# Kernel optimization log

Hardware: AMD Instinct MI355X
Metric: run time of the kernel (lower is better)

Reference implementation:

```python
import jax, jax.numpy as jnp
import numpy as np

RADIUS = 10  # watermark_radius
EPS = 1e-5   # BatchNorm eps

def _conv(x, w, b, g, be, m, v):
    # Conv2d 3x3 pad 1 + BatchNorm(eval) + ReLU, NCHW
    y = jax.lax.conv_general_dilated(x, w, (1, 1), 'SAME',
                                     dimension_numbers=('NCHW', 'OIHW', 'NCHW'))
    y = y + b[None, :, None, None]
    y = g[None, :, None, None] * (y - m[None, :, None, None]) * jax.lax.rsqrt(v + EPS)[None, :, None, None] + be[None, :, None, None]
    return jax.nn.relu(y)

def _watermark_indices(C, H, W, L, r):
    # Replicates the (channel, i, j) iteration order of the torch loop.
    chs, ys, xs = [], [], []
    cy0, cx0 = H // 2, W // 2
    for c in range(C):
        for i in range(-r, r + 1):
            for j in range(-r, r + 1):
                if len(chs) >= L:
                    return np.array(chs), np.array(ys), np.array(xs)
                y, x = cy0 + i, cx0 + j
                if 0 <= y < H and 0 <= x < W and i * i + j * j <= r * r:
                    chs.append(c); ys.append(y); xs.append(x)
    return np.array(chs), np.array(ys), np.array(xs)

def setup_inputs() -> dict:
    key = jax.random.key(0)
    ks = jax.random.split(key, 8)
    B, Cc, H, W, L = 16, 64, 256, 256, 256
    s = 0.05  # weight scale for numerical stability
    inp = {
        'image': jax.random.normal(ks[0], (B, 3, H, W), jnp.float32),
        'message': jax.random.uniform(ks[1], (B, L), jnp.float32),
        'w0': jax.random.normal(ks[2], (Cc, 3, 3, 3), jnp.float32) * s,
        'b0': jnp.zeros((Cc,), jnp.float32),
        'g0': jnp.ones((Cc,), jnp.float32),
        'be0': jnp.zeros((Cc,), jnp.float32),
        'm0': jnp.zeros((Cc,), jnp.float32),
        'v0': jnp.ones((Cc,), jnp.float32),
        'wk': jax.random.normal(ks[3], (3, Cc, Cc, 3, 3), jnp.float32) * s,
        'bk': jnp.zeros((3, Cc), jnp.float32),
        'gk': jnp.ones((3, Cc), jnp.float32),
        'bek': jnp.zeros((3, Cc), jnp.float32),
        'mk': jnp.zeros((3, Cc), jnp.float32),
        'vk': jnp.ones((3, Cc), jnp.float32),
        'wa': jax.random.normal(ks[4], (Cc, Cc + 3 + L, 3, 3), jnp.float32) * s,
        'ba': jnp.zeros((Cc,), jnp.float32),
        'ga': jnp.ones((Cc,), jnp.float32),
        'bea': jnp.zeros((Cc,), jnp.float32),
        'ma': jnp.zeros((Cc,), jnp.float32),
        'va': jnp.ones((Cc,), jnp.float32),
        'wf': jax.random.normal(ks[5], (3, Cc, 1, 1), jnp.float32) * s,
        'bf': jnp.zeros((3,), jnp.float32),
    }
    return inp

def reference(image, message, w0, b0, g0, be0, m0, v0,
              wk, bk, gk, bek, mk, vk,
              wa, ba, ga, bea, ma, va, wf, bf):
    B, _, H, W = image.shape
    L = message.shape[1]
    # conv stack
    x = _conv(image, w0, b0, g0, be0, m0, v0)
    for t in range(wk.shape[0]):
        x = _conv(x, wk[t], bk[t], gk[t], bek[t], mk[t], vk[t])
    C = x.shape[1]
    # FFT2 over spatial dims
    fft = jnp.fft.fft2(x.astype(jnp.complex64))
    # vectorized tree-ring watermark scatter (precomputed static indices)
    ch, yy, xx = _watermark_indices(C, H, W, L, RADIUS)
    vals = message[:, :ch.shape[0]]                      # [B, L]
    cvals = (vals + 1j * vals).astype(jnp.complex64)     # complex(value, value)
    fft = fft.at[:, ch, yy, xx].set(cvals)
    enc = jnp.fft.ifft2(fft).real.astype(image.dtype)
    # concat [expanded message, encoded, image]
    msg = jnp.broadcast_to(message[:, :, None, None], (B, L, H, W))
    cat = jnp.concatenate([msg, enc, image], axis=1)
    y = _conv(cat, wa, ba, ga, bea, ma, va)
    # final 1x1 conv
    out = jnp.einsum('bchw,oc->bohw', y, wf[:, :, 0, 0]) + bf[None, :, None, None]
    return out
```

## Files before the change

### kernel.cpp

```cpp
#include <hip/hip_runtime.h>
#include <hip/hip_bf16.h>

#define HH 256
#define WW 256
#define NB 16
#define CC 64
#define NL 256
#define HWSZ (HH*WW)
#define EPSV 1e-5f
#define NYK 16
#define YK0 118

using bf16 = __hip_bfloat16;
using short8  = __attribute__((ext_vector_type(8))) short;
using floatx4 = __attribute__((ext_vector_type(4))) float;

__device__ __forceinline__ ushort f2b(float f){
    bf16 h = __float2bfloat16(f);
    union { bf16 h; ushort u; } cv; cv.h = h; return cv.u;
}
__device__ __forceinline__ float b2fu(ushort u){
    union { unsigned int i; float f; } cv; cv.i = ((unsigned int)u) << 16; return cv.f;
}

__global__ void prep_w_k(const float* __restrict__ wk, const float* __restrict__ wa,
                         ushort* __restrict__ wkb2, ushort* __restrict__ wab2)
{
    int i = blockIdx.x*256 + threadIdx.x;
    const int NWK = 3*9*64*64, NWA = 19*2048;
    if (i < NWK) {
        int ci8 = i & 7; int r = i >> 3;
        int lane = r & 63; r >>= 6;
        int mi = r & 3; r >>= 2;
        int g = r % 18; int t = r / 18;
        int q = g / 6, kc2 = (g / 3) & 1, p = g % 3;
        int quad = lane >> 4, n16 = lane & 15;
        int co = mi*16 + n16, ci = kc2*32 + quad*8 + ci8, tap = p*3 + q;
        wkb2[i] = f2b(wk[(((size_t)t*64 + co)*64 + ci)*9 + tap]);
    } else if (i < NWK + NWA) {
        int i2 = i - NWK;
        int ci8 = i2 & 7; int r = i2 >> 3;
        int lane = r & 63; r >>= 6;
        int mi = r & 3; int g = r >> 2;
        int quad = lane >> 4, n16 = lane & 15;
        int co = mi*16 + n16;
        float v = 0.f;
        if (g < 18) {
            int q = g/6, kc2 = (g/3)&1, p = g%3;
            int ci = kc2*32 + quad*8 + ci8, tap = p*3 + q;
            v = wa[((size_t)co*323 + 256 + ci)*9 + tap];
        } else {
            int j = quad*8 + ci8;
            if (j < 27) {
                int ci = j/9, rem = j%9;
                v = wa[((size_t)co*323 + 320 + ci)*9 + rem];
            }
        }
        wab2[i2] = f2b(v);
    }
}

#define LDAF2(DST, G) { const ushort* bp = wbase + (size_t)(G)*2048;           \
    DST[0] = *(const short8*)(bp);                                             \
    DST[1] = *(const short8*)(bp + 512); }

#define MFMA_GRP2(AF, BF, P)                                                   \
    _Pragma("unroll") for (int mi_=0; mi_<2; mi_++) {                          \
      _Pragma("unroll") for (int ni_=0; ni_<4; ni_++)                          \
        acc[mi_][ni_] = __builtin_amdgcn_mfma_f32_16x16x32_bf16(               \
            AF[mi_], BF[ni_+(P)], acc[mi_][ni_], 0, 0, 0); }

__global__ __launch_bounds__(512,4) void conv0_k(
    const float* __restrict__ img, const float* __restrict__ w0,
    const float* __restrict__ bias, const float* __restrict__ gamma,
    const float* __restrict__ beta, const float* __restrict__ mean,
    const float* __restrict__ var, ushort* __restrict__ outp)
{
    __shared__ float s_i[3][18][18];
    __shared__ float s_wv[64*27];
    __shared__ float s_al[64], s_be[64];
    __shared__ ushort __align__(16) s_y[256*72];

    int tid = threadIdx.x;
    int x0 = blockIdx.x*16, y0 = blockIdx.y*16, b = blockIdx.z;
    if (tid < 64) {
        float a = gamma[tid]*rsqrtf(var[tid]+EPSV);
        s_al[tid] = a; s_be[tid] = (bias[tid]-mean[tid])*a + beta[tid];
    }
    for (int c = tid; c < 64*27; c += 512) s_wv[c] = w0[c];
    for (int c = tid; c < 3*18*18; c += 512) {
        int ci = c / 324, pp = c % 324, py = pp/18, px = pp%18;
        int gy = y0-1+py, gx = x0-1+px;
        float v = 0.f;
        if ((unsigned)gy < 256u && (unsigned)gx < 256u)
            v = img[((size_t)b*3 + ci)*HWSZ + gy*256 + gx];
        s_i[ci][py][px] = v;
    }
    __syncthreads();

    int px256 = tid & 255;
    int half  = tid >> 8;
    int ly = px256 >> 4, lx = px256 & 15;
    float xv[27];
    #pragma unroll
    for (int ci=0;ci<3;ci++)
      #pragma unroll
      for (int p=0;p<3;p++)
        #pragma unroll
        for (int q=0;q<3;q++)
            xv[ci*9+p*3+q] = s_i[ci][ly+p][lx+q];

    for (int cc=0; cc<32; cc++) {
        int co = half*32 + cc;
        float a = 0.f;
        #pragma unroll
        for (int j=0;j<27;j++) a += xv[j]*s_wv[co*27+j];
        s_y[px256*72 + co] = f2b(fmaxf(s_al[co]*a + s_be[co], 0.f));
    }
    __syncthreads();
    size_t obase = (size_t)b*HWSZ*64;
    for (int c = tid; c < 256*8; c += 512) {
        int ci8 = c & 7, px = c >> 3;
        int gy = y0 + (px>>4), gx = x0 + (px&15);
        *(uint4*)&outp[obase + (size_t)(gy*256+gx)*64 + ci8*8] =
            *(const uint4*)&s_y[px*72 + ci8*8];
    }
}

__global__ __launch_bounds__(512,4) void convm_k(
    const ushort* __restrict__ in, const ushort* __restrict__ wgt,
    ushort* __restrict__ outp,
    const float* __restrict__ gamma, const float* __restrict__ beta,
    const float* __restrict__ mean,  const float* __restrict__ var,
    const float* __restrict__ bias,  float* __restrict__ plane)
{
    __shared__ ushort __align__(16) s_x[18*18*72];
    __shared__ float s_al[64], s_be[64];

    const int tid = threadIdx.x;
    const int x0 = blockIdx.x*16, y0 = blockIdx.y*16, b = blockIdx.z;

    if (tid < 64) {
        float a = gamma[tid]*rsqrtf(var[tid]+EPSV);
        s_al[tid] = a; s_be[tid] = (bias[tid]-mean[tid])*a + beta[tid];
    }
    const size_t ibase = (size_t)b*HWSZ*64;
    for (int c = tid; c < 18*18*8; c += 512) {
        int ci8 = c & 7, pp = c >> 3;
        int px = pp % 18, py = pp / 18;
        int gy = y0-1+py, gx = x0-1+px;
        uint4 v = make_uint4(0,0,0,0);
        if ((unsigned)gy < 256u && (unsigned)gx < 256u)
            v = *(const uint4*)&in[ibase + (size_t)(gy*256+gx)*64 + ci8*8];
        *(uint4*)&s_x[(py*18+px)*72 + ci8*8] = v;
    }
    __syncthreads();

    const int lane = tid & 63, wv = tid >> 6;
    const int wid = wv & 3, grp = wv >> 2;
    const int n16 = lane & 15, quad = lane >> 4;
    const ushort* wbase = wgt + (size_t)lane*8 + (size_t)grp*1024;

    floatx4 acc[2][4];
    #pragma unroll
    for (int mi=0;mi<2;mi++)
      #pragma unroll
      for (int ni=0;ni<4;ni++)
        #pragma unroll
        for (int r=0;r<4;r++) acc[mi][ni][r] = 0.f;

    short8 afA[2], afB[2], bfA[6], bfB[6];

    LDAF2(afA, 0);
    #pragma unroll
    for (int rr=0; rr<6; rr++)
        bfA[rr] = *(const short8*)&s_x[((wid*4+rr)*18 + n16)*72 + quad*8];

    #pragma unroll
    for (int g=0; g<18; g++) {
        const int p = g % 3, j = g / 3;
        if (g+1 < 18) {
            if (g & 1) { LDAF2(afA, g+1); } else { LDAF2(afB, g+1); }
        }
        if (p == 0 && j+1 < 6) {
            const int nq = (j+1) >> 1, nk = (j+1) & 1;
            if (j & 1) {
                #pragma unroll
                for (int rr=0; rr<6; rr++)
                    bfA[rr] = *(const short8*)&s_x[((wid*4+rr)*18 + n16 + nq)*72 + nk*32 + quad*8];
            } else {
                #pragma unroll
                for (int rr=0; rr<6; rr++)
                    bfB[rr] = *(const short8*)&s_x[((wid*4+rr)*18 + n16 + nq)*72 + nk*32 + quad*8];
            }
        }
        if (g & 1) { if (j & 1) { MFMA_GRP2(afB, bfB, p) } else { MFMA_GRP2(afB, bfA, p) } }
        else       { if (j & 1) { MFMA_GRP2(afA, bfB, p) } else { MFMA_GRP2(afA, bfA, p) } }
    }
    __syncthreads();

    ushort* s_y = s_x;
    #pragma unroll
    for (int mi=0;mi<2;mi++)
      #pragma unroll
      for (int ni=0;ni<4;ni++) {
        int ami = grp*2 + mi;
        int px = (wid*4+ni)*16 + n16;
        int cob = ami*16 + quad*4;
        ushort u[4];
        #pragma unroll
        for (int r=0;r<4;r++) {
            float y = fmaxf(s_al[cob+r]*acc[mi][ni][r] + s_be[cob+r], 0.f);
            u[r] = f2b(y);
            if (plane && ami==0 && quad==0 && r==0)
                plane[(size_t)b*HWSZ + (y0+wid*4+ni)*256 + x0 + n16] = y;
        }
        uint2 pk; pk.x = (uint)u[0] | ((uint)u[1]<<16); pk.y = (uint)u[2] | ((uint)u[3]<<16);
        *(uint2*)&s_y[px*72 + cob] = pk;
      }
    __syncthreads();
    for (int c = tid; c < 256*8; c += 512) {
        int ci8 = c & 7, px = c >> 3;
        int gy = y0 + (px>>4), gx = x0 + (px&15);
        *(uint4*)&outp[ibase + (size_t)(gy*256+gx)*64 + ci8*8] =
            *(const uint4*)&s_y[px*72 + ci8*8];
    }
}

__global__ __launch_bounds__(512,4) void conva_k(
    const ushort* __restrict__ enc, const float* __restrict__ img,
    const float* __restrict__ dplane, const ushort* __restrict__ wgt,
    const float* __restrict__ gamma, const float* __restrict__ beta,
    const float* __restrict__ mean,  const float* __restrict__ var,
    const float* __restrict__ bias,
    const float* __restrict__ Tb,
    const float* __restrict__ wf, const float* __restrict__ bfv,
    float* __restrict__ outp)
{
    __shared__ ushort __align__(16) s_x[18*18*72];
    __shared__ float s_al[64], s_be[64];
    __shared__ float s_T[64*9];
    __shared__ float s_wf[3*64];
    __shared__ float s_bf[3];

    const int tid = threadIdx.x;
    const int x0 = blockIdx.x*16, y0 = blockIdx.y*16, b = blockIdx.z;

    if (tid < 64) {
        float a = gamma[tid]*rsqrtf(var[tid]+EPSV);
        s_al[tid] = a; s_be[tid] = (bias[tid]-mean[tid])*a + beta[tid];
    }
    if (tid < 192) s_wf[tid] = wf[tid];
    if (tid < 3)   s_bf[tid] = bfv[tid];
    for (int c = tid; c < 64*9; c += 512) s_T[c] = Tb[(size_t)b*576 + c];

    const int lane = tid & 63, wv = tid >> 6;
    const int wid = wv & 3, grp = wv >> 2;
    const int n16 = lane & 15, quad = lane >> 4;
    const ushort* wbase = wgt + (size_t)lane*8 + (size_t)grp*1024;

    const size_t ibase = (size_t)b*HWSZ*64;
    for (int c = tid; c < 18*18*8; c += 512) {
        int ci8 = c & 7, pp = c >> 3;
        int px = pp % 18, py = pp / 18;
        int gy = y0-1+py, gx = x0-1+px;
        uint4 v = make_uint4(0,0,0,0);
        if ((unsigned)gy < 256u && (unsigned)gx < 256u) {
            v = *(const uint4*)&enc[ibase + (size_t)(gy*256+gx)*64 + ci8*8];
            if (ci8 == 0) {
                float d = dplane[(size_t)b*HWSZ + gy*256 + gx];
                ushort nb = f2b(b2fu((ushort)(v.x & 0xffffu)) + d);
                v.x = (v.x & 0xffff0000u) | (uint)nb;
            }
        }
        *(uint4*)&s_x[(py*18+px)*72 + ci8*8] = v;
    }

    short8 bimg[4];
    #pragma unroll
    for (int ni=0; ni<4; ni++) {
        short8 t;
        #pragma unroll
        for (int ci8=0; ci8<8; ci8++) {
            int j = quad*8 + ci8;
            float v = 0.f;
            if (j < 27) {
                int ci = j/9, rem = j%9, p = rem/3, q = rem%3;
                int gy = y0 + wid*4 + ni + p - 1, gx = x0 + n16 + q - 1;
                if ((unsigned)gy < 256u && (unsigned)gx < 256u)
                    v = img[((size_t)b*3 + ci)*HWSZ + gy*256 + gx];
            }
            t[ci8] = (short)f2b(v);
        }
        bimg[ni] = t;
    }
    __syncthreads();

    floatx4 acc[2][4];
    #pragma unroll
    for (int mi=0;mi<2;mi++)
      #pragma unroll
      for (int ni=0;ni<4;ni++)
        #pragma unroll
        for (int r=0;r<4;r++) acc[mi][ni][r] = 0.f;

    short8 afA[2], afB[2], bf[6];

    LDAF2(afA, 0);
    #pragma unroll
    for (int g=0; g<18; g++) {
        const int p = g % 3, j = g / 3;
        if (g & 1) { LDAF2(afA, g+1); } else { LDAF2(afB, g+1); }
        if (p == 0) {
            const int nq = j >> 1, nk = j & 1;
            #pragma unroll
            for (int rr=0; rr<6; rr++)
                bf[rr] = *(const short8*)&s_x[((wid*4+rr)*18 + n16 + nq)*72 + nk*32 + quad*8];
        }
        if (g & 1) { MFMA_GRP2(afB, bf, p) } else { MFMA_GRP2(afA, bf, p) }
    }
    #pragma unroll
    for (int mi=0;mi<2;mi++)
      #pragma unroll
      for (int ni=0;ni<4;ni++)
        acc[mi][ni] = __builtin_amdgcn_mfma_f32_16x16x32_bf16(
            afA[mi], bimg[ni], acc[mi][ni], 0, 0, 0);

    float po[3][4];
    #pragma unroll
    for (int o=0;o<3;o++)
      #pragma unroll
      for (int ni=0;ni<4;ni++) po[o][ni] = 0.f;

    #pragma unroll
    for (int mi=0;mi<2;mi++) {
        int cob = (grp*2 + mi)*16 + quad*4;
        #pragma unroll
        for (int r=0;r<4;r++) {
            int co = cob + r;
            float al = s_al[co], be = s_be[co];
            const float* t = &s_T[co*9];
            float w0f = s_wf[0*64+co], w1f = s_wf[1*64+co], w2f = s_wf[2*64+co];
            #pragma unroll
            for (int ni=0;ni<4;ni++) {
                int h = y0 + wid*4 + ni, w = x0 + n16;
                float tv = t[0];
                if (h==0)   tv -= t[1];
                if (h==255) tv -= t[2];
                if (w==0)   tv -= t[3];
                if (w==255) tv -= t[4];
                if (h==0   && w==0)   tv += t[5];
                if (h==0   && w==255) tv += t[6];
                if (h==255 && w==0)   tv += t[7];
                if (h==255 && w==255) tv += t[8];
                float y = fmaxf(al*(acc[mi][ni][r] + tv) + be, 0.f);
                po[0][ni] += w0f*y; po[1][ni] += w1f*y; po[2][ni] += w2f*y;
            }
        }
    }
    #pragma unroll
    for (int o=0;o<3;o++)
      #pragma unroll
      for (int ni=0;ni<4;ni++) {
        po[o][ni] += __shfl_xor(po[o][ni], 16, 64);
        po[o][ni] += __shfl_xor(po[o][ni], 32, 64);
      }
    __syncthreads();
    float* s_red = (float*)s_x;
    #pragma unroll
    for (int o=0;o<3;o++)
      #pragma unroll
      for (int ni=0;ni<4;ni++)
        if (grp == 1 && quad == o)
            s_red[((wid*3+o)*4+ni)*16 + n16] = po[o][ni];
    __syncthreads();
    #pragma unroll
    for (int o=0;o<3;o++)
      #pragma unroll
      for (int ni=0;ni<4;ni++)
        if (grp == 0 && quad == o) {
            int h = y0 + wid*4 + ni, w = x0 + n16;
            outp[((size_t)b*3 + o)*HWSZ + h*256 + w] =
                po[o][ni] + s_red[((wid*3+o)*4+ni)*16 + n16] + s_bf[o];
        }
}

__global__ __launch_bounds__(256) void msgterm_k(const float* __restrict__ msg,
                                                 const float* __restrict__ wa,
                                                 float* __restrict__ Tbuf)
{
    __shared__ float red[256];
    int b = blockIdx.x, o = blockIdx.y, l = threadIdx.x;
    float m = msg[b*NL + l];
    float wv[9];
    #pragma unroll
    for (int t=0;t<9;t++) wv[t] = wa[((size_t)o*323 + l)*9 + t] * m;
    float comp[9];
    comp[0] = wv[0]+wv[1]+wv[2]+wv[3]+wv[4]+wv[5]+wv[6]+wv[7]+wv[8];
    comp[1] = wv[0]+wv[1]+wv[2];
    comp[2] = wv[6]+wv[7]+wv[8];
    comp[3] = wv[0]+wv[3]+wv[6];
    comp[4] = wv[2]+wv[5]+wv[8];
    comp[5] = wv[0]; comp[6]=wv[2]; comp[7]=wv[6]; comp[8]=wv[8];
    for (int cpi=0;cpi<9;cpi++){
        red[l] = comp[cpi];
        __syncthreads();
        for (int s=128;s>0;s>>=1){ if (l<s) red[l]+=red[l+s]; __syncthreads(); }
        if (l==0) Tbuf[((size_t)b*CC+o)*9+cpi] = red[0];
        __syncthreads();
    }
}

__global__ void build_idx_k(int* __restrict__ idx)
{
    if (threadIdx.x==0 && blockIdx.x==0) {
        int n=0;
        for (int i=-10;i<=10;i++)
            for (int j=-10;j<=10;j++) {
                if (n>=NL) return;
                if (i*i+j*j<=100) { idx[2*n]=128+i; idx[2*n+1]=128+j; n++; }
            }
    }
}

__global__ __launch_bounds__(256) void colA_k(const float* __restrict__ plane,
                                              float* __restrict__ Cbuf)
{
    __shared__ float twc[256], tws[256];
    int t = blockIdx.x, b = blockIdx.y, w = threadIdx.x;
    float sv, cv;
    __sincosf(6.283185307179586f * (float)w / 256.0f, &sv, &cv);
    twc[w]=cv; tws[w]=sv;
    __syncthreads();
    int yk = YK0 + t;
    const float* pb = &plane[(size_t)b*HWSZ];
    int m = 0;
    float fr=0.f, fi=0.f;
    for (int h=0; h<256; h++) {
        float xv = pb[h*256 + w];
        fr += xv*twc[m];
        fi -= xv*tws[m];
        m = (m + yk) & 255;
    }
    float* Cb = &Cbuf[((size_t)(b*NYK + t)*2)*256];
    Cb[w]       = fr;
    Cb[256 + w] = fi;
}

__global__ __launch_bounds__(256) void freqB_k(const float* __restrict__ Cbuf,
                                               const float* __restrict__ msg,
                                               const int* __restrict__ idx,
                                               float* __restrict__ D)
{
    __shared__ float twc[256], tws[256];
    __shared__ float sfr[4], sfi[4];
    int k = blockIdx.x, b = blockIdx.y, w = threadIdx.x;
    float sv, cv;
    __sincosf(6.283185307179586f * (float)w / 256.0f, &sv, &cv);
    twc[w]=cv; tws[w]=sv;
    __syncthreads();
    int yk = idx[2*k], xk = idx[2*k+1];
    int t = yk - YK0;
    const float* Cb = &Cbuf[((size_t)(b*NYK + t)*2)*256];
    float Cr = Cb[w], Ci = Cb[256 + w];
    int ang = (xk*w) & 255;
    float cx = twc[ang], sx = tws[ang];
    float fr = Cr*cx + Ci*sx;
    float fi = Ci*cx - Cr*sx;
    #pragma unroll
    for (int off=32; off>0; off>>=1) {
        fr += __shfl_xor(fr, off, 64);
        fi += __shfl_xor(fi, off, 64);
    }
    if ((w & 63) == 0) { sfr[w>>6] = fr; sfi[w>>6] = fi; }
    __syncthreads();
    if (w == 0) {
        float FR = sfr[0]+sfr[1]+sfr[2]+sfr[3];
        float FI = sfi[0]+sfi[1]+sfi[2]+sfi[3];
        float mv = msg[b*NL + k];
        D[((size_t)b*NL + k)*2 + 0] = mv - FR;
        D[((size_t)b*NL + k)*2 + 1] = mv - FI;
    }
}

__global__ __launch_bounds__(256) void rowC_k(const int* __restrict__ idx,
                                              const float* __restrict__ D,
                                              float* __restrict__ Sbuf)
{
    __shared__ float twc[256], tws[256], dr[256], di[256];
    __shared__ int iy[256], ix[256];
    int t = blockIdx.x, b = blockIdx.y, w = threadIdx.x;
    float sv, cv;
    __sincosf(6.283185307179586f * (float)w / 256.0f, &sv, &cv);
    twc[w]=cv; tws[w]=sv;
    dr[w] = D[((size_t)b*NL + w)*2+0];
    di[w] = D[((size_t)b*NL + w)*2+1];
    iy[w] = idx[2*w]; ix[w] = idx[2*w+1];
    __syncthreads();
    int yk = YK0 + t;
    float Sr=0.f, Si=0.f;
    for (int k=0;k<256;k++) {
        if (iy[k] != yk) continue;
        int ang = (ix[k]*w) & 255;
        float c = twc[ang], s = tws[ang];
        Sr += dr[k]*c - di[k]*s;
        Si += dr[k]*s + di[k]*c;
    }
    float* Sb = &Sbuf[((size_t)(b*NYK + t)*2)*256];
    Sb[w]       = Sr;
    Sb[256 + w] = Si;
}

__global__ __launch_bounds__(256) void applyD_k(const float* __restrict__ Sbuf,
                                                float* __restrict__ dplane)
{
    __shared__ float twc[256], tws[256];
    int h = blockIdx.x, b = blockIdx.y, w = threadIdx.x;
    float sv, cv;
    __sincosf(6.283185307179586f * (float)w / 256.0f, &sv, &cv);
    twc[w]=cv; tws[w]=sv;
    __syncthreads();
    float acc = 0.f;
    #pragma unroll
    for (int t=0;t<NYK;t++) {
        int yk = YK0 + t;
        int ang = (yk*h) & 255;
        float cy = twc[ang], sy = tws[ang];
        const float* Sb = &Sbuf[((size_t)(b*NYK + t)*2)*256];
        acc += cy*Sb[w] - sy*Sb[256 + w];
    }
    dplane[(size_t)b*HWSZ + h*256 + w] = acc * (1.0f/65536.0f);
}

extern "C" void kernel_launch(void* const* d_in, const int* in_sizes, int n_in,
                              void* d_out, int out_size, void* d_ws, size_t ws_size,
                              hipStream_t stream)
{
    const float* image = (const float*)d_in[0];
    const float* msg   = (const float*)d_in[1];
    const float* w0    = (const float*)d_in[2];
    const float* b0    = (const float*)d_in[3];
    const float* g0    = (const float*)d_in[4];
    const float* be0   = (const float*)d_in[5];
    const float* m0    = (const float*)d_in[6];
    const float* v0    = (const float*)d_in[7];
    const float* wk    = (const float*)d_in[8];
    const float* bk    = (const float*)d_in[9];
    const float* gk    = (const float*)d_in[10];
    const float* bek   = (const float*)d_in[11];
    const float* mk    = (const float*)d_in[12];
    const float* vk    = (const float*)d_in[13];
    const float* wa    = (const float*)d_in[14];
    const float* ba    = (const float*)d_in[15];
    const float* ga    = (const float*)d_in[16];
    const float* bea   = (const float*)d_in[17];
    const float* ma    = (const float*)d_in[18];
    const float* va    = (const float*)d_in[19];
    const float* wf    = (const float*)d_in[20];
    const float* bfv   = (const float*)d_in[21];
    float* out = (float*)d_out;

    char* base = (char*)d_ws;
    int*    idx    = (int*)base;
    float*  Dbuf   = (float*)(base + (4<<10));
    float*  Tbuf   = (float*)(base + (40<<10));
    ushort* wkb2   = (ushort*)(base + (128<<10));
    ushort* wab2   = (ushort*)(base + (384<<10));
    float*  Cbuf   = (float*)(base + (512<<10));
    float*  Sbuf   = (float*)(base + ((size_t)1<<20));
    float*  plane  = (float*)(base + ((size_t)2<<20));
    float*  dplane = (float*)(base + ((size_t)7<<20));
    ushort* bufA   = (ushort*)(base + ((size_t)12<<20));

    const size_t perB = (size_t)HWSZ*64*2*2;
    int chunk = 1;
    for (int c = NB; c >= 1; c >>= 1)
        if (((size_t)12<<20) + (size_t)c*perB <= ws_size) { chunk = c; break; }
    ushort* bufB = bufA + (size_t)chunk*HWSZ*64;

    build_idx_k<<<1,64,0,stream>>>(idx);
    msgterm_k<<<dim3(NB,CC),256,0,stream>>>(msg, wa, Tbuf);
    int prep_n = (3*9*64*64 + 19*2048 + 255)/256;
    prep_w_k<<<prep_n,256,0,stream>>>(wk, wa, wkb2, wab2);

    const size_t WL = (size_t)9*64*64;

    for (int cs = 0; cs < NB; cs += chunk) {
        dim3 g(16,16,chunk);
        const float* img_c = image + (size_t)cs*3*HWSZ;

        conv0_k<<<g,512,0,stream>>>(img_c, w0, b0, g0, be0, m0, v0, bufA);
        convm_k<<<g,512,0,stream>>>(bufA, wkb2 + 0*WL, bufB,
            gk+0*CC, bek+0*CC, mk+0*CC, vk+0*CC, bk+0*CC, nullptr);
        convm_k<<<g,512,0,stream>>>(bufB, wkb2 + 1*WL, bufA,
            gk+1*CC, bek+1*CC, mk+1*CC, vk+1*CC, bk+1*CC, nullptr);
        convm_k<<<g,512,0,stream>>>(bufA, wkb2 + 2*WL, bufB,
            gk+2*CC, bek+2*CC, mk+2*CC, vk+2*CC, bk+2*CC, plane);

        colA_k<<<dim3(NYK,chunk),256,0,stream>>>(plane, Cbuf);
        freqB_k<<<dim3(NL,chunk),256,0,stream>>>(Cbuf, msg + (size_t)cs*NL, idx, Dbuf);
        rowC_k<<<dim3(NYK,chunk),256,0,stream>>>(idx, Dbuf, Sbuf);
        applyD_k<<<dim3(HH,chunk),256,0,stream>>>(Sbuf, dplane);

        conva_k<<<g,512,0,stream>>>(bufB, img_c, dplane, wab2,
            ga, bea, ma, va, ba, Tbuf + (size_t)cs*CC*9, wf, bfv,
            out + (size_t)cs*3*HWSZ);
    }
}
```

Measured before the change: 780.4 us.

## Split convm halo load into two channel halves and overlap with MFMA

The convm kernel now loads only the first 32 input channels of the halo tile into LDS before starting compute. The upper 32 channels are prefetched into registers and written to LDS during the first MFMA group. The K-loop order is remapped (GMAP) so the low-channel taps run first, with a barrier at step 6 before the high-channel taps. Halo loads and output stores are also unrolled, and conva_k gets a fast path for interior tiles that skips the border correction terms. This aims to hide global load latency behind MFMA work, at the cost of extra registers for the staged data and an additional barrier.

```diff
diff --git a/kernel.cpp b/kernel.cpp
--- a/kernel.cpp
+++ b/kernel.cpp
@@ -70,6 +70,8 @@
         acc[mi_][ni_] = __builtin_amdgcn_mfma_f32_16x16x32_bf16(               \
             AF[mi_], BF[ni_+(P)], acc[mi_][ni_], 0, 0, 0); }
 
+#define GMAP(G) ((((G)%9)/3)*6 + ((G)/9)*3 + ((G)%3))
+
 __global__ __launch_bounds__(512,4) void conv0_k(
     const float* __restrict__ img, const float* __restrict__ w0,
     const float* __restrict__ bias, const float* __restrict__ gamma,
@@ -145,16 +147,45 @@
         s_al[tid] = a; s_be[tid] = (bias[tid]-mean[tid])*a + beta[tid];
     }
     const size_t ibase = (size_t)b*HWSZ*64;
-    for (int c = tid; c < 18*18*8; c += 512) {
-        int ci8 = c & 7, pp = c >> 3;
+
+    {
+        int c = tid;
+        int ci4 = c & 3; int pp = c >> 2;
         int px = pp % 18, py = pp / 18;
-        int gy = y0-1+py, gx = x0-1+px;
-        uint4 v = make_uint4(0,0,0,0);
-        if ((unsigned)gy < 256u && (unsigned)gx < 256u)
-            v = *(const uint4*)&in[ibase + (size_t)(gy*256+gx)*64 + ci8*8];
-        *(uint4*)&s_x[(py*18+px)*72 + ci8*8] = v;
-    }
-    __syncthreads();
+        #pragma unroll
+        for (int it = 0; it < 3; ++it) {
+            if (c < 1296) {
+                int gy = y0-1+py, gx = x0-1+px;
+                uint4 v = make_uint4(0,0,0,0);
+                if ((unsigned)gy < 256u && (unsigned)gx < 256u)
+                    v = *(const uint4*)&in[ibase + (size_t)(gy*256+gx)*64 + ci4*8];
+                *(uint4*)&s_x[pp*72 + ci4*8] = v;
+            }
+            c += 512; pp += 128; px += 2; py += 7;
+            if (px >= 18) { px -= 18; py += 1; }
+        }
+    }
+    uint4 stgHi[3];
+    {
+        int c = tid;
+        int ci4 = c & 3; int pp = c >> 2;
+        int px = pp % 18, py = pp / 18;
+        #pragma unroll
+        for (int it = 0; it < 3; ++it) {
+            uint4 v = make_uint4(0,0,0,0);
+            if (c < 1296) {
+                int gy = y0-1+py, gx = x0-1+px;
+                if ((unsigned)gy < 256u && (unsigned)gx < 256u)
+                    v = *(const uint4*)&in[ibase + (size_t)(gy*256+gx)*64 + 32 + ci4*8];
+            }
+            stgHi[it] = v;
+            c += 512; pp += 128; px += 2; py += 7;
+            if (px >= 18) { px -= 18; py += 1; }
+        }
+    }
+    asm volatile("s_waitcnt lgkmcnt(0)" ::: "memory");
+    __builtin_amdgcn_s_barrier();
+    __builtin_amdgcn_sched_barrier(0);
 
     const int lane = tid & 63, wv = tid >> 6;
     const int wid = wv & 3, grp = wv >> 2;
@@ -171,31 +202,44 @@
 
     short8 afA[2], afB[2], bfA[6], bfB[6];
 
-    LDAF2(afA, 0);
+    LDAF2(afA, GMAP(0));
     #pragma unroll
     for (int rr=0; rr<6; rr++)
         bfA[rr] = *(const short8*)&s_x[((wid*4+rr)*18 + n16)*72 + quad*8];
 
     #pragma unroll
-    for (int g=0; g<18; g++) {
-        const int p = g % 3, j = g / 3;
-        if (g+1 < 18) {
-            if (g & 1) { LDAF2(afA, g+1); } else { LDAF2(afB, g+1); }
-        }
-        if (p == 0 && j+1 < 6) {
-            const int nq = (j+1) >> 1, nk = (j+1) & 1;
-            if (j & 1) {
+    for (int gg=0; gg<18; ++gg) {
+        const int p = gg % 3, jp = gg / 3;
+        if (gg == 6) {
+            asm volatile("s_waitcnt lgkmcnt(0)" ::: "memory");
+            __builtin_amdgcn_s_barrier();
+            __builtin_amdgcn_sched_barrier(0);
+        }
+        if (gg + 1 < 18) {
+            if (gg & 1) { LDAF2(afA, GMAP(gg+1)); } else { LDAF2(afB, GMAP(gg+1)); }
+        }
+        if (p == 0 && jp + 1 < 6) {
+            const int kn = (jp+1) / 3, qn = (jp+1) % 3;
+            if (jp & 1) {
                 #pragma unroll
                 for (int rr=0; rr<6; rr++)
-                    bfA[rr] = *(const short8*)&s_x[((wid*4+rr)*18 + n16 + nq)*72 + nk*32 + quad*8];
+                    bfA[rr] = *(const short8*)&s_x[((wid*4+rr)*18 + n16 + qn)*72 + kn*32 + quad*8];
             } else {
                 #pragma unroll
                 for (int rr=0; rr<6; rr++)
-                    bfB[rr] = *(const short8*)&s_x[((wid*4+rr)*18 + n16 + nq)*72 + nk*32 + quad*8];
-            }
-        }
-        if (g & 1) { if (j & 1) { MFMA_GRP2(afB, bfB, p) } else { MFMA_GRP2(afB, bfA, p) } }
-        else       { if (j & 1) { MFMA_GRP2(afA, bfB, p) } else { MFMA_GRP2(afA, bfA, p) } }
+                    bfB[rr] = *(const short8*)&s_x[((wid*4+rr)*18 + n16 + qn)*72 + kn*32 + quad*8];
+            }
+        }
+        if (gg == 0) {
+            int c = tid; int ci4 = c & 3; int pp = c >> 2;
+            #pragma unroll
+            for (int it = 0; it < 3; ++it) {
+                if (c < 1296) *(uint4*)&s_x[pp*72 + 32 + ci4*8] = stgHi[it];
+                c += 512; pp += 128;
+            }
+        }
+        if (gg & 1) { if (jp & 1) { MFMA_GRP2(afB, bfB, p) } else { MFMA_GRP2(afB, bfA, p) } }
+        else        { if (jp & 1) { MFMA_GRP2(afA, bfB, p) } else { MFMA_GRP2(afA, bfA, p) } }
     }
     __syncthreads();
 
@@ -219,11 +263,16 @@
         *(uint2*)&s_y[px*72 + cob] = pk;
       }
     __syncthreads();
-    for (int c = tid; c < 256*8; c += 512) {
+    {
+        int c = tid;
         int ci8 = c & 7, px = c >> 3;
         int gy = y0 + (px>>4), gx = x0 + (px&15);
-        *(uint4*)&outp[ibase + (size_t)(gy*256+gx)*64 + ci8*8] =
-            *(const uint4*)&s_y[px*72 + ci8*8];
+        #pragma unroll
+        for (int it = 0; it < 4; ++it) {
+            *(uint4*)&outp[ibase + (size_t)(gy*256+gx)*64 + ci8*8] =
+                *(const uint4*)&s_y[px*72 + ci8*8];
+            px += 64; gy += 4;
+        }
     }
 }
 
@@ -260,20 +309,28 @@
     const ushort* wbase = wgt + (size_t)lane*8 + (size_t)grp*1024;
 
     const size_t ibase = (size_t)b*HWSZ*64;
-    for (int c = tid; c < 18*18*8; c += 512) {
-        int ci8 = c & 7, pp = c >> 3;
+    {
+        int c = tid;
+        int ci8 = c & 7; int pp = c >> 3;
         int px = pp % 18, py = pp / 18;
-        int gy = y0-1+py, gx = x0-1+px;
-        uint4 v = make_uint4(0,0,0,0);
-        if ((unsigned)gy < 256u && (unsigned)gx < 256u) {
-            v = *(const uint4*)&enc[ibase + (size_t)(gy*256+gx)*64 + ci8*8];
-            if (ci8 == 0) {
-                float d = dplane[(size_t)b*HWSZ + gy*256 + gx];
-                ushort nb = f2b(b2fu((ushort)(v.x & 0xffffu)) + d);
-                v.x = (v.x & 0xffff0000u) | (uint)nb;
-            }
-        }
-        *(uint4*)&s_x[(py*18+px)*72 + ci8*8] = v;
+        #pragma unroll
+        for (int it = 0; it < 6; ++it) {
+            if (c < 2592) {
+                int gy = y0-1+py, gx = x0-1+px;
+                uint4 v = make_uint4(0,0,0,0);
+                if ((unsigned)gy < 256u && (unsigned)gx < 256u) {
+                    v = *(const uint4*)&enc[ibase + (size_t)(gy*256+gx)*64 + ci8*8];
+                    if (ci8 == 0) {
+                        float d = dplane[(size_t)b*HWSZ + gy*256 + gx];
+                        ushort nb = f2b(b2fu((ushort)(v.x & 0xffffu)) + d);
+                        v.x = (v.x & 0xffff0000u) | (uint)nb;
+                    }
+                }
+                *(uint4*)&s_x[pp*72 + ci8*8] = v;
+            }
+            c += 512; pp += 64; px += 10; py += 3;
+            if (px >= 18) { px -= 18; py += 1; }
+        }
     }
 
     short8 bimg[4];
@@ -332,6 +389,8 @@
       #pragma unroll
       for (int ni=0;ni<4;ni++) po[o][ni] = 0.f;
 
+    const bool interior = (x0 != 0) && (x0 != 240) && (y0 != 0) && (y0 != 240);
+
     #pragma unroll
     for (int mi=0;mi<2;mi++) {
         int cob = (grp*2 + mi)*16 + quad*4;
@@ -341,20 +400,29 @@
             float al = s_al[co], be = s_be[co];
             const float* t = &s_T[co*9];
             float w0f = s_wf[0*64+co], w1f = s_wf[1*64+co], w2f = s_wf[2*64+co];
-            #pragma unroll
-            for (int ni=0;ni<4;ni++) {
-                int h = y0 + wid*4 + ni, w = x0 + n16;
+            if (interior) {
                 float tv = t[0];
-                if (h==0)   tv -= t[1];
-                if (h==255) tv -= t[2];
-                if (w==0)   tv -= t[3];
-                if (w==255) tv -= t[4];
-                if (h==0   && w==0)   tv += t[5];
-                if (h==0   && w==255) tv += t[6];
-                if (h==255 && w==0)   tv += t[7];
-                if (h==255 && w==255) tv += t[8];
-                float y = fmaxf(al*(acc[mi][ni][r] + tv) + be, 0.f);
-                po[0][ni] += w0f*y; po[1][ni] += w1f*y; po[2][ni] += w2f*y;
+                #pragma unroll
+                for (int ni=0;ni<4;ni++) {
+                    float y = fmaxf(al*(acc[mi][ni][r] + tv) + be, 0.f);
+                    po[0][ni] += w0f*y; po[1][ni] += w1f*y; po[2][ni] += w2f*y;
+                }
+            } else {
+                #pragma unroll
+                for (int ni=0;ni<4;ni++) {
+                    int h = y0 + wid*4 + ni, w = x0 + n16;
+                    float tv = t[0];
+                    if (h==0)   tv -= t[1];
+                    if (h==255) tv -= t[2];
+                    if (w==0)   tv -= t[3];
+                    if (w==255) tv -= t[4];
+                    if (h==0   && w==0)   tv += t[5];
+                    if (h==0   && w==255) tv += t[6];
+                    if (h==255 && w==0)   tv += t[7];
+                    if (h==255 && w==255) tv += t[8];
+                    float y = fmaxf(al*(acc[mi][ni][r] + tv) + be, 0.f);
+                    po[0][ni] += w0f*y; po[1][ni] += w1f*y; po[2][ni] += w2f*y;
+                }
             }
         }
     }
```

After: 783.8 us. Within noise of the previous version (+0.4%).

## Load conv halo tiles via direct global-to-LDS with XOR-swizzled layout

Applied to the files above, without the earlier changes.

The 64-channel conv kernel now stages interior halo tiles with global_load_lds, which writes 16 bytes straight into LDS without a register round trip. The LDS row stride drops from a padded 72 to 64 elements, and an XOR swizzle on the 8-element channel groups avoids bank conflicts. The B-fragment reads and the output staging are rewritten to use the swizzled layout, and edge tiles keep a guarded register path. The final conv kernel's loops are unrolled and it skips the border-correction branches for interior tiles.

```diff
diff --git a/kernel.cpp b/kernel.cpp
--- a/kernel.cpp
+++ b/kernel.cpp
@@ -21,6 +21,13 @@
 }
 __device__ __forceinline__ float b2fu(ushort u){
     union { unsigned int i; float f; } cv; cv.i = ((unsigned int)u) << 16; return cv.f;
+}
+
+__device__ __forceinline__ void gload_lds16(const ushort* gsrc, ushort* lbase){
+    __builtin_amdgcn_global_load_lds(
+        (const __attribute__((address_space(1))) unsigned int*)(const void*)gsrc,
+        (__attribute__((address_space(3))) unsigned int*)(void*)lbase,
+        16, 0, 0);
 }
 
 __global__ void prep_w_k(const float* __restrict__ wk, const float* __restrict__ wa,
@@ -134,7 +141,7 @@
     const float* __restrict__ mean,  const float* __restrict__ var,
     const float* __restrict__ bias,  float* __restrict__ plane)
 {
-    __shared__ ushort __align__(16) s_x[18*18*72];
+    __shared__ ushort __align__(16) s_x[18*18*64];
     __shared__ float s_al[64], s_be[64];
 
     const int tid = threadIdx.x;
@@ -145,18 +152,43 @@
         s_al[tid] = a; s_be[tid] = (bias[tid]-mean[tid])*a + beta[tid];
     }
     const size_t ibase = (size_t)b*HWSZ*64;
-    for (int c = tid; c < 18*18*8; c += 512) {
-        int ci8 = c & 7, pp = c >> 3;
-        int px = pp % 18, py = pp / 18;
-        int gy = y0-1+py, gx = x0-1+px;
-        uint4 v = make_uint4(0,0,0,0);
-        if ((unsigned)gy < 256u && (unsigned)gx < 256u)
-            v = *(const uint4*)&in[ibase + (size_t)(gy*256+gx)*64 + ci8*8];
-        *(uint4*)&s_x[(py*18+px)*72 + ci8*8] = v;
-    }
-    __syncthreads();
-
     const int lane = tid & 63, wv = tid >> 6;
+
+    const bool interior = (x0 != 0) && (x0 != 240) && (y0 != 0) && (y0 != 240);
+    if (interior) {
+        #pragma unroll
+        for (int it = 0; it < 5; ++it) {
+            int cbase = (wv*5 + it)*64;
+            int s = cbase + lane;
+            int pp = s >> 3, gs = s & 7;
+            int gl = gs ^ (pp & 7);
+            int py = pp/18, px = pp - py*18;
+            const ushort* src = &in[ibase + (size_t)((y0-1+py)*256 + (x0-1+px))*64 + gl*8];
+            gload_lds16(src, &s_x[cbase*8]);
+        }
+        if (wv == 0) {
+            int cbase = 2528;
+            int s = cbase + lane;
+            int pp = s >> 3, gs = s & 7;
+            int gl = gs ^ (pp & 7);
+            int py = pp/18, px = pp - py*18;
+            const ushort* src = &in[ibase + (size_t)((y0-1+py)*256 + (x0-1+px))*64 + gl*8];
+            gload_lds16(src, &s_x[cbase*8]);
+        }
+    } else {
+        for (int c = tid; c < 2592; c += 512) {
+            int pp = c >> 3, gl = c & 7;
+            int sg = gl ^ (pp & 7);
+            int py = pp/18, px = pp - py*18;
+            int gy = y0-1+py, gx = x0-1+px;
+            uint4 v = make_uint4(0,0,0,0);
+            if ((unsigned)gy < 256u && (unsigned)gx < 256u)
+                v = *(const uint4*)&in[ibase + (size_t)(gy*256+gx)*64 + gl*8];
+            *(uint4*)&s_x[pp*64 + sg*8] = v;
+        }
+    }
+    __syncthreads();
+
     const int wid = wv & 3, grp = wv >> 2;
     const int n16 = lane & 15, quad = lane >> 4;
     const ushort* wbase = wgt + (size_t)lane*8 + (size_t)grp*1024;
@@ -173,8 +205,10 @@
 
     LDAF2(afA, 0);
     #pragma unroll
-    for (int rr=0; rr<6; rr++)
-        bfA[rr] = *(const short8*)&s_x[((wid*4+rr)*18 + n16)*72 + quad*8];
+    for (int rr=0; rr<6; rr++) {
+        int row = (wid*4+rr)*18 + n16;
+        bfA[rr] = *(const short8*)&s_x[row*64 + ((quad ^ (row&7)))*8];
+    }
 
     #pragma unroll
     for (int g=0; g<18; g++) {
@@ -186,12 +220,16 @@
             const int nq = (j+1) >> 1, nk = (j+1) & 1;
             if (j & 1) {
                 #pragma unroll
-                for (int rr=0; rr<6; rr++)
-                    bfA[rr] = *(const short8*)&s_x[((wid*4+rr)*18 + n16 + nq)*72 + nk*32 + quad*8];
+                for (int rr=0; rr<6; rr++) {
+                    int row = (wid*4+rr)*18 + n16 + nq;
+                    bfA[rr] = *(const short8*)&s_x[row*64 + (((nk*4+quad) ^ (row&7)))*8];
+                }
             } else {
                 #pragma unroll
-                for (int rr=0; rr<6; rr++)
-                    bfB[rr] = *(const short8*)&s_x[((wid*4+rr)*18 + n16 + nq)*72 + nk*32 + quad*8];
+                for (int rr=0; rr<6; rr++) {
+                    int row = (wid*4+rr)*18 + n16 + nq;
+                    bfB[rr] = *(const short8*)&s_x[row*64 + (((nk*4+quad) ^ (row&7)))*8];
+                }
             }
         }
         if (g & 1) { if (j & 1) { MFMA_GRP2(afB, bfB, p) } else { MFMA_GRP2(afB, bfA, p) } }
@@ -216,14 +254,20 @@
                 plane[(size_t)b*HWSZ + (y0+wid*4+ni)*256 + x0 + n16] = y;
         }
         uint2 pk; pk.x = (uint)u[0] | ((uint)u[1]<<16); pk.y = (uint)u[2] | ((uint)u[3]<<16);
-        *(uint2*)&s_y[px*72 + cob] = pk;
+        int gl = cob >> 3, sub = quad & 1;
+        *(uint2*)&s_y[px*64 + ((gl ^ (px&7)))*8 + sub*4] = pk;
       }
     __syncthreads();
-    for (int c = tid; c < 256*8; c += 512) {
+    {
+        int c = tid;
         int ci8 = c & 7, px = c >> 3;
         int gy = y0 + (px>>4), gx = x0 + (px&15);
-        *(uint4*)&outp[ibase + (size_t)(gy*256+gx)*64 + ci8*8] =
-            *(const uint4*)&s_y[px*72 + ci8*8];
+        #pragma unroll
+        for (int it = 0; it < 4; ++it) {
+            *(uint4*)&outp[ibase + (size_t)(gy*256+gx)*64 + ci8*8] =
+                *(const uint4*)&s_y[px*64 + ((ci8 ^ (px&7)))*8];
+            px += 64; gy += 4;
+        }
     }
 }
 
@@ -260,20 +304,28 @@
     const ushort* wbase = wgt + (size_t)lane*8 + (size_t)grp*1024;
 
     const size_t ibase = (size_t)b*HWSZ*64;
-    for (int c = tid; c < 18*18*8; c += 512) {
-        int ci8 = c & 7, pp = c >> 3;
+    {
+        int c = tid;
+        int ci8 = c & 7; int pp = c >> 3;
         int px = pp % 18, py = pp / 18;
-        int gy = y0-1+py, gx = x0-1+px;
-        uint4 v = make_uint4(0,0,0,0);
-        if ((unsigned)gy < 256u && (unsigned)gx < 256u) {
-            v = *(const uint4*)&enc[ibase + (size_t)(gy*256+gx)*64 + ci8*8];
-            if (ci8 == 0) {
-                float d = dplane[(size_t)b*HWSZ + gy*256 + gx];
-                ushort nb = f2b(b2fu((ushort)(v.x & 0xffffu)) + d);
-                v.x = (v.x & 0xffff0000u) | (uint)nb;
+        #pragma unroll
+        for (int it = 0; it < 6; ++it) {
+            if (c < 2592) {
+                int gy = y0-1+py, gx = x0-1+px;
+                uint4 v = make_uint4(0,0,0,0);
+                if ((unsigned)gy < 256u && (unsigned)gx < 256u) {
+                    v = *(const uint4*)&enc[ibase + (size_t)(gy*256+gx)*64 + ci8*8];
+                    if (ci8 == 0) {
+                        float d = dplane[(size_t)b*HWSZ + gy*256 + gx];
+                        ushort nb = f2b(b2fu((ushort)(v.x & 0xffffu)) + d);
+                        v.x = (v.x & 0xffff0000u) | (uint)nb;
+                    }
+                }
+                *(uint4*)&s_x[pp*72 + ci8*8] = v;
             }
-        }
-        *(uint4*)&s_x[(py*18+px)*72 + ci8*8] = v;
+            c += 512; pp += 64; px += 10; py += 3;
+            if (px >= 18) { px -= 18; py += 1; }
+        }
     }
 
     short8 bimg[4];
@@ -332,6 +384,8 @@
       #pragma unroll
       for (int ni=0;ni<4;ni++) po[o][ni] = 0.f;
 
+    const bool interior = (x0 != 0) && (x0 != 240) && (y0 != 0) && (y0 != 240);
+
     #pragma unroll
     for (int mi=0;mi<2;mi++) {
         int cob = (grp*2 + mi)*16 + quad*4;
@@ -341,20 +395,29 @@
             float al = s_al[co], be = s_be[co];
             const float* t = &s_T[co*9];
             float w0f = s_wf[0*64+co], w1f = s_wf[1*64+co], w2f = s_wf[2*64+co];
-            #pragma unroll
-            for (int ni=0;ni<4;ni++) {
-                int h = y0 + wid*4 + ni, w = x0 + n16;
+            if (interior) {
                 float tv = t[0];
-                if (h==0)   tv -= t[1];
-                if (h==255) tv -= t[2];
-                if (w==0)   tv -= t[3];
-                if (w==255) tv -= t[4];
-                if (h==0   && w==0)   tv += t[5];
-                if (h==0   && w==255) tv += t[6];
-                if (h==255 && w==0)   tv += t[7];
-                if (h==255 && w==255) tv += t[8];
-                float y = fmaxf(al*(acc[mi][ni][r] + tv) + be, 0.f);
-                po[0][ni] += w0f*y; po[1][ni] += w1f*y; po[2][ni] += w2f*y;
+                #pragma unroll
+                for (int ni=0;ni<4;ni++) {
+                    float y = fmaxf(al*(acc[mi][ni][r] + tv) + be, 0.f);
+                    po[0][ni] += w0f*y; po[1][ni] += w1f*y; po[2][ni] += w2f*y;
+                }
+            } else {
+                #pragma unroll
+                for (int ni=0;ni<4;ni++) {
+                    int h = y0 + wid*4 + ni, w = x0 + n16;
+                    float tv = t[0];
+                    if (h==0)   tv -= t[1];
+                    if (h==255) tv -= t[2];
+                    if (w==0)   tv -= t[3];
+                    if (w==255) tv -= t[4];
+                    if (h==0   && w==0)   tv += t[5];
+                    if (h==0   && w==255) tv += t[6];
+                    if (h==255 && w==0)   tv += t[7];
+                    if (h==255 && w==255) tv += t[8];
+                    float y = fmaxf(al*(acc[mi][ni][r] + tv) + be, 0.f);
+                    po[0][ni] += w0f*y; po[1][ni] += w1f*y; po[2][ni] += w2f*y;
+                }
             }
         }
     }
```

New measurement: 785.4 us. Within noise of the previous version (+0.6%).
